# Kernel optimization log

Measured on AMD Instinct MI355X. Metric: run time of the kernel, lower is better.

## Reference

```python
import jax, jax.numpy as jnp
import numpy as np

_SAMPLING_EPS = 1e-05
_RMAX = 0.9999999403953552          # largest float32 uniform from tl.rand
_RMAX_LOG = -5.960464477539063e-08  # log(_RMAX)


def setup_inputs() -> dict:
    key = jax.random.key(0)
    k1, k2, k3, k4, k5 = jax.random.split(key, 5)
    B, V = 256, 128000
    logits = jax.random.normal(k1, (B, V), dtype=jnp.float32) * 4.0
    temperature = jax.random.uniform(k2, (B,), dtype=jnp.float32, minval=0.1, maxval=1.5)
    top_k = jax.random.randint(k3, (B,), 1, 1000).astype(jnp.int32)
    top_p = jax.random.uniform(k4, (B,), dtype=jnp.float32, minval=0.5, maxval=1.0)
    gumbel_u = jax.random.uniform(k5, (B, V), dtype=jnp.float32)
    return {
        "logits": logits,
        "temperature": temperature,
        "top_k": top_k,
        "top_p": top_p,
        "gumbel_u": gumbel_u,
        "num_logprobs": 20,
    }


def reference(logits, temperature, top_k, top_p, gumbel_u, num_logprobs):
    B, V = logits.shape
    # --- apply_temperature: divide by temp, temp<eps treated as 1.0 (greedy) ---
    temp = jnp.where(temperature < _SAMPLING_EPS, 1.0, temperature)
    logits = logits.astype(jnp.float32) / temp[:, None]

    # --- apply_top_k_top_p: sort ascending, mask, scatter back ---
    idx_sort = jnp.argsort(logits, axis=-1)                      # ascending
    logits_sort = jnp.take_along_axis(logits, idx_sort, axis=-1)
    # top-k: value of the k-th largest is at position V-k in ascending order
    k_pos = (V - top_k.astype(jnp.int32))[:, None]
    thresh = jnp.take_along_axis(logits_sort, k_pos, axis=-1)    # [B,1]
    logits_sort = jnp.where(logits_sort < thresh, -jnp.inf, logits_sort)
    # top-p: drop ascending prefix whose cumulative prob <= 1-p (keep last)
    probs_sort = jax.nn.softmax(logits_sort, axis=-1)
    cum = jnp.cumsum(probs_sort, axis=-1)
    mask_p = cum <= (1.0 - top_p)[:, None]
    mask_p = mask_p.at[:, -1].set(False)
    logits_sort = jnp.where(mask_p, -jnp.inf, logits_sort)
    # unsort back to vocab order
    inv = jnp.argsort(idx_sort, axis=-1)
    logits_f = jnp.take_along_axis(logits_sort, inv, axis=-1)

    # --- softmax + gumbel-trick sampling: argmax(p / -log(u)) ---
    probs = jax.nn.softmax(logits_f, axis=-1)
    q = -jnp.where(gumbel_u >= _RMAX, _RMAX_LOG, jnp.log(gumbel_u))
    greedy = (temperature < _SAMPLING_EPS)[:, None]  # kernel skips these rows
    ratio = jnp.where(greedy, probs, probs / q)
    sampled = jnp.argmax(ratio, axis=-1)             # [B]

    # --- gather_logprobs ---
    logprobs = jax.nn.log_softmax(logits_f, axis=-1)
    sampled_lp = jnp.take_along_axis(logprobs, sampled[:, None], axis=-1)  # [B,1]
    ranks = jnp.sum(logprobs > sampled_lp, axis=-1)                        # [B]
    topk_lp, topk_idx = jax.lax.top_k(logprobs, num_logprobs)
    indices = jnp.concatenate([sampled[:, None], topk_idx], axis=1)        # [B,1+K]
    lp_vals = jnp.concatenate([sampled_lp, topk_lp], axis=1)               # [B,1+K]

    return sampled[:, None], indices, lp_vals, ranks
```

## Files before the change

kernel.cpp:

```cpp
#include <hip/hip_runtime.h>
#include <math.h>

#define NTHR 1024
#define CAP 4096
#define BINS 4096

#define RMAX_F 0.9999999403953552f
#define RMAX_LOG_F -5.960464477539063e-08f
#define NEG_BIG -3.0e38f

__device__ __forceinline__ unsigned keyOf(float v) {
    unsigned b = __float_as_uint(v);
    return (b & 0x80000000u) ? ~b : (b | 0x80000000u);
}
__device__ __forceinline__ float valOfKey(unsigned k) {
    unsigned b = (k & 0x80000000u) ? (k ^ 0x80000000u) : ~k;
    return __uint_as_float(b);
}

__global__ __launch_bounds__(NTHR) void sampler_kernel(
    const float* __restrict__ logits,
    const float* __restrict__ temperature,
    const int* __restrict__ top_kv,
    const float* __restrict__ top_pv,
    const float* __restrict__ gumbel,
    float* __restrict__ out,
    int B, int V, int K)
{
    const int r = blockIdx.x;
    const int tid = threadIdx.x;
    const int lane = tid & 63;

    __shared__ unsigned long long cand[CAP];
    __shared__ int scanI[NTHR];
    __shared__ float varr[1024];
    __shared__ float Earr[1024];
    __shared__ float sfx[1024];
    __shared__ unsigned char flagArr[1024];
    __shared__ unsigned bitmap[64];
    __shared__ unsigned s_tlo;
    __shared__ int s_fallback;
    __shared__ unsigned s_prefix;
    __shared__ int s_cntgt, s_total, s_lvl;
    __shared__ int s_ncand, s_nkeep, s_rank, s_g0, s_g1;
    __shared__ unsigned long long s_amax;
    __shared__ float s_vs;

    unsigned* hist = (unsigned*)cand;

    const float* row = logits + (long long)r * V;
    const float* urow = gumbel + (long long)r * V;

    float traw = temperature[r];
    bool greedy = traw < 1e-5f;
    float t = greedy ? 1.0f : traw;
    int k = top_kv[r];
    if (k < 1) k = 1;
    if (k > V) k = V;
    float p = top_pv[r];

    const float4* row4 = (const float4*)row;
    const int V4 = V >> 2;
    const int Vt = V4 << 2;
    const unsigned cpy = tid & 1u;

    auto procF4 = [&](float4 l4, int i4) {
        float vv[4] = { l4.x, l4.y, l4.z, l4.w };
        #pragma unroll
        for (int j = 0; j < 4; ++j) {
            unsigned key = keyOf(vv[j]);
            bool pred = (key >= s_tlo);
            unsigned long long mask = __ballot(pred ? 1 : 0);
            if (mask) {
                int leader = __ffsll(mask) - 1;
                int cnt = __popcll(mask);
                int base = 0;
                if (lane == leader) base = atomicAdd(&s_ncand, cnt);
                base = __shfl(base, leader);
                if (pred) {
                    int pos = base + __popcll(mask & ((1ULL << lane) - 1ULL));
                    if (pos < CAP) {
                        unsigned gidx = (unsigned)(i4 * 4 + j);
                        cand[pos] = ((unsigned long long)key << 32) | (unsigned)(~gidx);
                    }
                }
            }
        }
    };
    auto compact = [&]() {
        int i = tid;
        for (; i + 3 * NTHR < V4; i += 4 * NTHR) {
            float4 a0 = row4[i];
            float4 a1 = row4[i + NTHR];
            float4 a2 = row4[i + 2 * NTHR];
            float4 a3 = row4[i + 3 * NTHR];
            procF4(a0, i); procF4(a1, i + NTHR);
            procF4(a2, i + 2 * NTHR); procF4(a3, i + 3 * NTHR);
        }
        for (; i < V4; i += NTHR) { float4 a = row4[i]; procF4(a, i); }
        for (int j = Vt + tid; j < V; j += NTHR) {
            unsigned key = keyOf(row[j]);
            bool pred = (key >= s_tlo);
            unsigned long long mask = __ballot(pred ? 1 : 0);
            if (mask) {
                int leader = __ffsll(mask) - 1;
                int cnt = __popcll(mask);
                int base = 0;
                if (lane == leader) base = atomicAdd(&s_ncand, cnt);
                base = __shfl(base, leader);
                if (pred) {
                    int pos = base + __popcll(mask & ((1ULL << lane) - 1ULL));
                    if (pos < CAP)
                        cand[pos] = ((unsigned long long)key << 32) | (unsigned)(~(unsigned)j);
                }
            }
        }
    };

    for (int i = tid; i < BINS * 2; i += NTHR) hist[i] = 0;
    __syncthreads();
    for (int i = tid; i < V4; i += NTHR * 8) {
        float4 l4 = row4[i];
        atomicAdd(&hist[((keyOf(l4.x) >> 20) << 1) | cpy], 1u);
        atomicAdd(&hist[((keyOf(l4.y) >> 20) << 1) | cpy], 1u);
        atomicAdd(&hist[((keyOf(l4.z) >> 20) << 1) | cpy], 1u);
        atomicAdd(&hist[((keyOf(l4.w) >> 20) << 1) | cpy], 1u);
    }
    __syncthreads();
    {
        int base = tid << 2;
        int cs = 0;
        #pragma unroll
        for (int j = 0; j < 4; ++j)
            cs += (int)(hist[(base + j) * 2] + hist[(base + j) * 2 + 1]);
        scanI[tid] = cs;
    }
    __syncthreads();
    for (int d = 1; d < NTHR; d <<= 1) {
        int v = (tid + d < NTHR) ? scanI[tid + d] : 0;
        __syncthreads();
        scanI[tid] += v;
        __syncthreads();
    }
    const int S = scanI[0];
    long long ks = ((long long)k * S) / V;
    const int starg = (int)ks + 40 + (int)(ks >> 2);
    if (tid == 0) s_fallback = (2 * starg > S) ? 1 : 0;
    __syncthreads();
    if (!s_fallback) {
        int mine = scanI[tid];
        int above = (tid + 1 < NTHR) ? scanI[tid + 1] : 0;
        if (mine >= starg && above < starg) {
            int base = tid << 2;
            int run = above;
            for (int b = base + 3; b >= base; --b) {
                int mb = (int)(hist[b * 2] + hist[b * 2 + 1]);
                if (run + mb >= starg) { s_tlo = (unsigned)b << 20; break; }
                run += mb;
            }
        }
        __syncthreads();
        if (tid == 0) s_ncand = 0;
        __syncthreads();
        compact();
        __syncthreads();
        if (tid == 0) s_fallback = (s_ncand < k || s_ncand > CAP) ? 1 : 0;
    }
    __syncthreads();

    if (s_fallback) {
        for (int i = tid; i < BINS * 2; i += NTHR) hist[i] = 0;
        __syncthreads();
        for (int i = tid; i < V4; i += NTHR) {
            float4 l4 = row4[i];
            atomicAdd(&hist[((keyOf(l4.x) >> 20) << 1) | cpy], 1u);
            atomicAdd(&hist[((keyOf(l4.y) >> 20) << 1) | cpy], 1u);
            atomicAdd(&hist[((keyOf(l4.z) >> 20) << 1) | cpy], 1u);
            atomicAdd(&hist[((keyOf(l4.w) >> 20) << 1) | cpy], 1u);
        }
        for (int i = Vt + tid; i < V; i += NTHR)
            atomicAdd(&hist[((keyOf(row[i]) >> 20) << 1) | cpy], 1u);
        __syncthreads();
        {
            int base = tid << 2;
            int cs = 0;
            #pragma unroll
            for (int j = 0; j < 4; ++j)
                cs += (int)(hist[(base + j) * 2] + hist[(base + j) * 2 + 1]);
            scanI[tid] = cs;
        }
        __syncthreads();
        for (int d = 1; d < NTHR; d <<= 1) {
            int v = (tid + d < NTHR) ? scanI[tid + d] : 0;
            __syncthreads();
            scanI[tid] += v;
            __syncthreads();
        }
        {
            int mine = scanI[tid];
            int above = (tid + 1 < NTHR) ? scanI[tid + 1] : 0;
            if (mine >= k && above < k) {
                int base = tid << 2;
                int run = above;
                for (int b = base + 3; b >= base; --b) {
                    int mb = (int)(hist[b * 2] + hist[b * 2 + 1]);
                    if (run + mb >= k) {
                        s_prefix = (unsigned)b; s_cntgt = run;
                        s_total = run + mb; s_lvl = 0;
                        break;
                    }
                    run += mb;
                }
            }
        }
        for (int level = 1; level <= 2; ++level) {
            __syncthreads();
            if (s_total <= CAP) break;
            for (int i = tid; i < 512; i += NTHR) hist[i] = 0;
            __syncthreads();
            unsigned pfx = s_prefix;
            const int msh = 32 - (12 + 8 * (level - 1));
            const int bsh = msh - 8;
            for (int i = tid; i < V4; i += NTHR) {
                float4 l4 = row4[i];
                float vv[4] = { l4.x, l4.y, l4.z, l4.w };
                #pragma unroll
                for (int j = 0; j < 4; ++j) {
                    unsigned key = keyOf(vv[j]);
                    if ((key >> msh) == pfx)
                        atomicAdd(&hist[(((key >> bsh) & 255u) << 1) | cpy], 1u);
                }
            }
            for (int i = Vt + tid; i < V; i += NTHR) {
                unsigned key = keyOf(row[i]);
                if ((key >> msh) == pfx)
                    atomicAdd(&hist[(((key >> bsh) & 255u) << 1) | cpy], 1u);
            }
            __syncthreads();
            if (tid == 0) {
                int run = s_cntgt;
                for (int b = 255; b >= 0; --b) {
                    int mb = (int)(hist[b * 2] + hist[b * 2 + 1]);
                    if (run + mb >= k) {
                        s_prefix = (pfx << 8) | (unsigned)b;
                        s_cntgt = run; s_total = run + mb;
                        break;
                    }
                    run += mb;
                }
                s_lvl = level;
            }
        }
        __syncthreads();
        if (tid == 0) { s_tlo = s_prefix << (20 - 8 * s_lvl); s_ncand = 0; }
        __syncthreads();
        compact();
        __syncthreads();
    }

    int ncand = s_ncand; if (ncand > CAP) ncand = CAP;
    if (k > ncand) k = ncand;

    int P = 2; while (P < ncand) P <<= 1;
    for (int i = ncand + tid; i < P; i += NTHR) cand[i] = 0ULL;
    __syncthreads();
    for (int size = 2; size <= P; size <<= 1) {
        for (int stride = size >> 1; stride > 0; stride >>= 1) {
            for (int i = tid; i < P; i += NTHR) {
                int j = i ^ stride;
                if (j > i) {
                    unsigned long long a = cand[i], b = cand[j];
                    bool up = ((i & size) == 0);
                    bool sw = up ? (a < b) : (a > b);
                    if (sw) { cand[i] = b; cand[j] = a; }
                }
            }
            __syncthreads();
        }
    }

    for (int i = tid; i < 1024; i += NTHR)
        varr[i] = (i < ncand) ? (valOfKey((unsigned)(cand[i] >> 32)) / t) : NEG_BIG;
    __syncthreads();

    const float m = varr[0];
    const float tkeyV = varr[k - 1];
    int ntop = k;
    while (ntop < ncand) {
        float vi = (ntop < 1024) ? varr[ntop]
                                 : (valOfKey((unsigned)(cand[ntop] >> 32)) / t);
        if (vi != tkeyV) break;
        ++ntop;
    }
    if (ntop > 1024) ntop = 1024;

    for (int i = tid; i < 1024; i += NTHR) {
        float e = (i < ntop) ? expf(varr[i] - m) : 0.0f;
        Earr[i] = e;
        sfx[i] = e;
    }
    __syncthreads();
    for (int d = 1; d < 1024; d <<= 1) {
        float t0 = (tid + d < 1024) ? sfx[tid + d] : 0.0f;
        __syncthreads();
        sfx[tid] += t0;
        __syncthreads();
    }
    const float Zp = sfx[0];
    const float cmp = 1.0f - p;
    if (tid == 0) { s_nkeep = 0; s_rank = 0; s_amax = 0ULL; }
    for (int i = tid; i < 64; i += NTHR) bitmap[i] = 0;
    __syncthreads();
    {
        int local = 0;
        for (int i = tid; i < ntop; i += NTHR)
            if (sfx[i] / Zp > cmp) local++;
        if (local) atomicAdd(&s_nkeep, local);
    }
    __syncthreads();
    const int nkeep = s_nkeep;
    if (tid == 0) {
        float vb = varr[nkeep - 1];
        int g0 = nkeep - 1;
        while (g0 > 0 && varr[g0 - 1] == vb) --g0;
        int g1 = nkeep;
        while (g1 < ntop && varr[g1] == vb) ++g1;
        s_g0 = g0; s_g1 = g1;
    }
    __syncthreads();
    const int g0 = s_g0, g1 = s_g1;
    const int mkeep = nkeep - g0;
    for (int i = g0 + tid; i < g1; i += NTHR) {
        unsigned gi = ~(unsigned)(cand[i] & 0xFFFFFFFFull);
        int rk = 0;
        for (int j = g0; j < g1; ++j) {
            unsigned gj = ~(unsigned)(cand[j] & 0xFFFFFFFFull);
            if (gj > gi) rk++;
        }
        flagArr[i] = (rk < mkeep) ? 1 : 0;
    }
    __syncthreads();

    const float Z2 = (nkeep < 1024) ? (Zp - sfx[nkeep]) : Zp;
    const float L = logf(Z2);

    for (int i = tid; i < g1; i += NTHR) {
        if (i < g0 || flagArr[i]) {
            unsigned lo = (unsigned)(cand[i] & 0xFFFFFFFFull);
            unsigned gidx = ~lo;
            float u = urow[gidx];
            float q = -((u >= RMAX_F) ? RMAX_LOG_F : logf(u));
            float prob = Earr[i] / Z2;
            float ratio = greedy ? prob : (prob / q);
            unsigned long long comp = ((unsigned long long)__float_as_uint(ratio) << 32) | lo;
            atomicMax(&s_amax, comp);
            if (gidx < 2048) atomicOr(&bitmap[gidx >> 5], 1u << (gidx & 31));
        }
    }
    __syncthreads();
    const unsigned samp_lo = (unsigned)(s_amax & 0xFFFFFFFFull);
    const unsigned samp = ~samp_lo;
    for (int i = tid; i < ntop; i += NTHR)
        if ((unsigned)(cand[i] & 0xFFFFFFFFull) == samp_lo) s_vs = varr[i];
    __syncthreads();
    const float lp_s = (s_vs - m) - L;
    {
        int local = 0;
        for (int i = tid; i < nkeep; i += NTHR)
            if ((varr[i] - m) - L > lp_s) local++;
        if (local) atomicAdd(&s_rank, local);
    }
    __syncthreads();

    if (tid == 0) {
        float* o_samp = out;
        float* o_idx  = out + B;
        float* o_lp   = out + B + (long long)B * (K + 1);
        float* o_rank = out + B + 2LL * B * (K + 1);
        long long rowo = (long long)r * (K + 1);

        o_samp[r] = (float)samp;
        o_idx[rowo] = (float)samp;
        o_lp[rowo] = lp_s;
        o_rank[r] = (float)s_rank;

        int ntk = (nkeep < K) ? nkeep : K;
        int slot = 0, i = 0;
        while (slot < ntk && i < g1) {
            float v = varr[i];
            int re = i + 1;
            while (re < g1 && varr[re] == v) ++re;
            long long last = -1;
            while (slot < ntk) {
                unsigned best = 0xFFFFFFFFu;
                for (int j = i; j < re; ++j) {
                    if (j >= g0 && !flagArr[j]) continue;
                    unsigned gj = ~(unsigned)(cand[j] & 0xFFFFFFFFull);
                    if ((long long)gj > last && gj < best) best = gj;
                }
                if (best == 0xFFFFFFFFu) break;
                o_idx[rowo + 1 + slot] = (float)best;
                o_lp[rowo + 1 + slot] = (v - m) - L;
                last = best; ++slot;
            }
            i = re;
        }
        if (nkeep < K) {
            int j = 0;
            for (int c = nkeep; c < K; ++c) {
                while (bitmap[j >> 5] & (1u << (j & 31))) ++j;
                o_idx[rowo + 1 + c] = (float)j;
                o_lp[rowo + 1 + c] = NEG_BIG;
                ++j;
            }
        }
    }
}

extern "C" void kernel_launch(void* const* d_in, const int* in_sizes, int n_in,
                              void* d_out, int out_size, void* d_ws, size_t ws_size,
                              hipStream_t stream) {
    const float* logits      = (const float*)d_in[0];
    const float* temperature = (const float*)d_in[1];
    const int*   top_k       = (const int*)d_in[2];
    const float* top_p       = (const float*)d_in[3];
    const float* gumbel      = (const float*)d_in[4];
    int B = in_sizes[1];
    int V = in_sizes[0] / B;
    int K = (out_size / B - 4) / 2;
    sampler_kernel<<<B, NTHR, 0, stream>>>(logits, temperature, top_k, top_p,
                                           gumbel, (float*)d_out, B, V, K);
}
```

Before: 323.2 us.

## Split sampler into threshold, multi-block compaction, and final kernels

Splits the single per-row kernel into three launches: a sampled histogram that estimates a per-row threshold, a candidate compaction spread over 8 blocks per row that writes to a global workspace through global atomics, and a final kernel that loads the candidates and does the sort, top-p, sampling and logprobs. The goal is to parallelise the full-row scan, which dominates the time, across more blocks than the 256 rows provide, so more CUs stream memory at once. It adds two extra launches, workspace traffic and global atomics, and falls back to the in-block path when the workspace is too small or the candidate count is off.

```diff
diff --git a/kernel.cpp b/kernel.cpp
--- a/kernel.cpp
+++ b/kernel.cpp
@@ -1,9 +1,12 @@
 #include <hip/hip_runtime.h>
 #include <math.h>
 
-#define NTHR 1024
+#define BINS 4096
 #define CAP 4096
-#define BINS 4096
+#define G 8
+#define NT1 1024
+#define NT2 256
+#define NT3 1024
 
 #define RMAX_F 0.9999999403953552f
 #define RMAX_LOG_F -5.960464477539063e-08f
@@ -18,28 +21,151 @@
     return __uint_as_float(b);
 }
 
-__global__ __launch_bounds__(NTHR) void sampler_kernel(
+__global__ __launch_bounds__(NT1) void k_thresh(
+    const float* __restrict__ logits, const int* __restrict__ top_kv,
+    unsigned* __restrict__ tloA, int* __restrict__ cntA, int V)
+{
+    const int r = blockIdx.x;
+    const int tid = threadIdx.x;
+    __shared__ unsigned hist[BINS * 2];
+    __shared__ int scanI[NT1];
+    __shared__ unsigned s_tlo;
+
+    const float* row = logits + (long long)r * V;
+    int k = top_kv[r];
+    if (k < 1) k = 1;
+    if (k > V) k = V;
+    const float4* row4 = (const float4*)row;
+    const int V4 = V >> 2;
+    const unsigned cpy = tid & 1u;
+
+    for (int i = tid; i < BINS * 2; i += NT1) hist[i] = 0;
+    if (tid == 0) s_tlo = 0u;
+    __syncthreads();
+    for (int i = tid; i < V4; i += NT1 * 8) {
+        float4 l4 = row4[i];
+        atomicAdd(&hist[((keyOf(l4.x) >> 20) << 1) | cpy], 1u);
+        atomicAdd(&hist[((keyOf(l4.y) >> 20) << 1) | cpy], 1u);
+        atomicAdd(&hist[((keyOf(l4.z) >> 20) << 1) | cpy], 1u);
+        atomicAdd(&hist[((keyOf(l4.w) >> 20) << 1) | cpy], 1u);
+    }
+    __syncthreads();
+    {
+        int base = tid << 2;
+        int cs = 0;
+        #pragma unroll
+        for (int j = 0; j < 4; ++j)
+            cs += (int)(hist[(base + j) * 2] + hist[(base + j) * 2 + 1]);
+        scanI[tid] = cs;
+    }
+    __syncthreads();
+    for (int d = 1; d < NT1; d <<= 1) {
+        int v = (tid + d < NT1) ? scanI[tid + d] : 0;
+        __syncthreads();
+        scanI[tid] += v;
+        __syncthreads();
+    }
+    const int S = scanI[0];
+    long long ks = ((long long)k * S) / V;
+    const int starg = (int)ks + 40 + (int)(ks >> 2);
+    const bool ok = (starg >= 1) && (2 * starg <= S);
+    if (ok) {
+        int mine = scanI[tid];
+        int above = (tid + 1 < NT1) ? scanI[tid + 1] : 0;
+        if (mine >= starg && above < starg) {
+            int base = tid << 2;
+            int run = above;
+            for (int b = base + 3; b >= base; --b) {
+                int mb = (int)(hist[b * 2] + hist[b * 2 + 1]);
+                if (run + mb >= starg) { s_tlo = (unsigned)b << 20; break; }
+                run += mb;
+            }
+        }
+    }
+    __syncthreads();
+    if (tid == 0) { tloA[r] = s_tlo; cntA[r] = 0; }
+}
+
+__global__ __launch_bounds__(NT2) void k_compact(
+    const float* __restrict__ logits, const unsigned* __restrict__ tloA,
+    int* __restrict__ cntA, unsigned long long* __restrict__ candg,
+    int V, int capws)
+{
+    const int gb = blockIdx.x;
+    const int r = gb >> 3;
+    const int s = gb & 7;
+    const int tid = threadIdx.x;
+    const int lane = tid & 63;
+
+    const float* row = logits + (long long)r * V;
+    const unsigned tlo = tloA[r];
+    int* cnt = &cntA[r];
+    unsigned long long* cbase = candg + (long long)r * capws;
+    const float4* row4 = (const float4*)row;
+    const int V4 = V >> 2;
+    const int Vt = V4 << 2;
+
+    auto emit = [&](unsigned key, unsigned gidx) {
+        bool pred = (key >= tlo);
+        unsigned long long mask = __ballot(pred ? 1 : 0);
+        if (mask) {
+            int leader = __ffsll(mask) - 1;
+            int c = __popcll(mask);
+            int base = 0;
+            if (lane == leader) base = atomicAdd(cnt, c);
+            base = __shfl(base, leader);
+            if (pred) {
+                int pos = base + __popcll(mask & ((1ULL << lane) - 1ULL));
+                if (pos < capws)
+                    cbase[pos] = ((unsigned long long)key << 32) | (unsigned)(~gidx);
+            }
+        }
+    };
+    auto procF4 = [&](float4 l4, int i4) {
+        emit(keyOf(l4.x), (unsigned)(i4 * 4 + 0));
+        emit(keyOf(l4.y), (unsigned)(i4 * 4 + 1));
+        emit(keyOf(l4.z), (unsigned)(i4 * 4 + 2));
+        emit(keyOf(l4.w), (unsigned)(i4 * 4 + 3));
+    };
+
+    const int stride = NT2 * G;
+    int i = s * NT2 + tid;
+    for (; i + 3 * stride < V4; i += 4 * stride) {
+        float4 a0 = row4[i];
+        float4 a1 = row4[i + stride];
+        float4 a2 = row4[i + 2 * stride];
+        float4 a3 = row4[i + 3 * stride];
+        procF4(a0, i); procF4(a1, i + stride);
+        procF4(a2, i + 2 * stride); procF4(a3, i + 3 * stride);
+    }
+    for (; i < V4; i += stride) { float4 a = row4[i]; procF4(a, i); }
+    if (s == 0)
+        for (int j = Vt + tid; j < V; j += NT2) emit(keyOf(row[j]), (unsigned)j);
+}
+
+__global__ __launch_bounds__(NT3) void k_final(
     const float* __restrict__ logits,
     const float* __restrict__ temperature,
     const int* __restrict__ top_kv,
     const float* __restrict__ top_pv,
     const float* __restrict__ gumbel,
+    const unsigned long long* __restrict__ candg,
+    const int* __restrict__ cntA,
     float* __restrict__ out,
-    int B, int V, int K)
+    int B, int V, int K, int capws)
 {
     const int r = blockIdx.x;
     const int tid = threadIdx.x;
     const int lane = tid & 63;
 
     __shared__ unsigned long long cand[CAP];
-    __shared__ int scanI[NTHR];
+    __shared__ int scanI[NT3];
     __shared__ float varr[1024];
     __shared__ float Earr[1024];
     __shared__ float sfx[1024];
     __shared__ unsigned char flagArr[1024];
     __shared__ unsigned bitmap[64];
     __shared__ unsigned s_tlo;
-    __shared__ int s_fallback;
     __shared__ unsigned s_prefix;
     __shared__ int s_cntgt, s_total, s_lvl;
     __shared__ int s_ncand, s_nkeep, s_rank, s_g0, s_g1;
@@ -64,41 +190,125 @@
     const int Vt = V4 << 2;
     const unsigned cpy = tid & 1u;
 
-    auto procF4 = [&](float4 l4, int i4) {
-        float vv[4] = { l4.x, l4.y, l4.z, l4.w };
-        #pragma unroll
-        for (int j = 0; j < 4; ++j) {
-            unsigned key = keyOf(vv[j]);
-            bool pred = (key >= s_tlo);
-            unsigned long long mask = __ballot(pred ? 1 : 0);
-            if (mask) {
-                int leader = __ffsll(mask) - 1;
-                int cnt = __popcll(mask);
-                int base = 0;
-                if (lane == leader) base = atomicAdd(&s_ncand, cnt);
-                base = __shfl(base, leader);
-                if (pred) {
-                    int pos = base + __popcll(mask & ((1ULL << lane) - 1ULL));
-                    if (pos < CAP) {
-                        unsigned gidx = (unsigned)(i4 * 4 + j);
-                        cand[pos] = ((unsigned long long)key << 32) | (unsigned)(~gidx);
+    const int ncand0 = cntA[r];
+    const bool fb = (ncand0 < k) || (ncand0 > capws);
+    int ncand;
+
+    if (!fb) {
+        const unsigned long long* cbase = candg + (long long)r * capws;
+        for (int i = tid; i < ncand0; i += NT3) cand[i] = cbase[i];
+        ncand = ncand0;
+    } else {
+        for (int i = tid; i < BINS * 2; i += NT3) hist[i] = 0;
+        __syncthreads();
+        for (int i = tid; i < V4; i += NT3) {
+            float4 l4 = row4[i];
+            atomicAdd(&hist[((keyOf(l4.x) >> 20) << 1) | cpy], 1u);
+            atomicAdd(&hist[((keyOf(l4.y) >> 20) << 1) | cpy], 1u);
+            atomicAdd(&hist[((keyOf(l4.z) >> 20) << 1) | cpy], 1u);
+            atomicAdd(&hist[((keyOf(l4.w) >> 20) << 1) | cpy], 1u);
+        }
+        for (int i = Vt + tid; i < V; i += NT3)
+            atomicAdd(&hist[((keyOf(row[i]) >> 20) << 1) | cpy], 1u);
+        __syncthreads();
+        {
+            int base = tid << 2;
+            int cs = 0;
+            #pragma unroll
+            for (int j = 0; j < 4; ++j)
+                cs += (int)(hist[(base + j) * 2] + hist[(base + j) * 2 + 1]);
+            scanI[tid] = cs;
+        }
+        __syncthreads();
+        for (int d = 1; d < NT3; d <<= 1) {
+            int v = (tid + d < NT3) ? scanI[tid + d] : 0;
+            __syncthreads();
+            scanI[tid] += v;
+            __syncthreads();
+        }
+        {
+            int mine = scanI[tid];
+            int above = (tid + 1 < NT3) ? scanI[tid + 1] : 0;
+            if (mine >= k && above < k) {
+                int base = tid << 2;
+                int run = above;
+                for (int b = base + 3; b >= base; --b) {
+                    int mb = (int)(hist[b * 2] + hist[b * 2 + 1]);
+                    if (run + mb >= k) {
+                        s_prefix = (unsigned)b; s_cntgt = run;
+                        s_total = run + mb; s_lvl = 0;
+                        break;
                     }
-                }
-            }
-        }
-    };
-    auto compact = [&]() {
-        int i = tid;
-        for (; i + 3 * NTHR < V4; i += 4 * NTHR) {
-            float4 a0 = row4[i];
-            float4 a1 = row4[i + NTHR];
-            float4 a2 = row4[i + 2 * NTHR];
-            float4 a3 = row4[i + 3 * NTHR];
-            procF4(a0, i); procF4(a1, i + NTHR);
-            procF4(a2, i + 2 * NTHR); procF4(a3, i + 3 * NTHR);
-        }
-        for (; i < V4; i += NTHR) { float4 a = row4[i]; procF4(a, i); }
-        for (int j = Vt + tid; j < V; j += NTHR) {
+                    run += mb;
+                }
+            }
+        }
+        for (int level = 1; level <= 2; ++level) {
+            __syncthreads();
+            if (s_total <= CAP) break;
+            for (int i = tid; i < 512; i += NT3) hist[i] = 0;
+            __syncthreads();
+            unsigned pfx = s_prefix;
+            const int msh = 32 - (12 + 8 * (level - 1));
+            const int bsh = msh - 8;
+            for (int i = tid; i < V4; i += NT3) {
+                float4 l4 = row4[i];
+                float vv[4] = { l4.x, l4.y, l4.z, l4.w };
+                #pragma unroll
+                for (int j = 0; j < 4; ++j) {
+                    unsigned key = keyOf(vv[j]);
+                    if ((key >> msh) == pfx)
+                        atomicAdd(&hist[(((key >> bsh) & 255u) << 1) | cpy], 1u);
+                }
+            }
+            for (int i = Vt + tid; i < V; i += NT3) {
+                unsigned key = keyOf(row[i]);
+                if ((key >> msh) == pfx)
+                    atomicAdd(&hist[(((key >> bsh) & 255u) << 1) | cpy], 1u);
+            }
+            __syncthreads();
+            if (tid == 0) {
+                int run = s_cntgt;
+                for (int b = 255; b >= 0; --b) {
+                    int mb = (int)(hist[b * 2] + hist[b * 2 + 1]);
+                    if (run + mb >= k) {
+                        s_prefix = (pfx << 8) | (unsigned)b;
+                        s_cntgt = run; s_total = run + mb;
+                        break;
+                    }
+                    run += mb;
+                }
+                s_lvl = level;
+            }
+        }
+        __syncthreads();
+        if (tid == 0) { s_tlo = s_prefix << (20 - 8 * s_lvl); s_ncand = 0; }
+        __syncthreads();
+        for (int i = tid; i < V4; i += NT3) {
+            float4 l4 = row4[i];
+            float vv[4] = { l4.x, l4.y, l4.z, l4.w };
+            #pragma unroll
+            for (int j = 0; j < 4; ++j) {
+                unsigned key = keyOf(vv[j]);
+                bool pred = (key >= s_tlo);
+                unsigned long long mask = __ballot(pred ? 1 : 0);
+                if (mask) {
+                    int leader = __ffsll(mask) - 1;
+                    int cnt = __popcll(mask);
+                    int base = 0;
+                    if (lane == leader) base = atomicAdd(&s_ncand, cnt);
+                    base = __shfl(base, leader);
+                    if (pred) {
+                        int pos = base + __popcll(mask & ((1ULL << lane) - 1ULL));
+                        if (pos < CAP) {
+                            unsigned gidx = (unsigned)(i * 4 + j);
+                            cand[pos] = ((unsigned long long)key << 32) | (unsigned)(~gidx);
+                        }
+                    }
+                }
+            }
+        }
+        for (int j = Vt + tid; j < V; j += NT3) {
             unsigned key = keyOf(row[j]);
             bool pred = (key >= s_tlo);
             unsigned long long mask = __ballot(pred ? 1 : 0);
@@ -115,158 +325,18 @@
                 }
             }
         }
-    };
-
-    for (int i = tid; i < BINS * 2; i += NTHR) hist[i] = 0;
-    __syncthreads();
-    for (int i = tid; i < V4; i += NTHR * 8) {
-        float4 l4 = row4[i];
-        atomicAdd(&hist[((keyOf(l4.x) >> 20) << 1) | cpy], 1u);
-        atomicAdd(&hist[((keyOf(l4.y) >> 20) << 1) | cpy], 1u);
-        atomicAdd(&hist[((keyOf(l4.z) >> 20) << 1) | cpy], 1u);
-        atomicAdd(&hist[((keyOf(l4.w) >> 20) << 1) | cpy], 1u);
-    }
-    __syncthreads();
-    {
-        int base = tid << 2;
-        int cs = 0;
-        #pragma unroll
-        for (int j = 0; j < 4; ++j)
-            cs += (int)(hist[(base + j) * 2] + hist[(base + j) * 2 + 1]);
-        scanI[tid] = cs;
-    }
-    __syncthreads();
-    for (int d = 1; d < NTHR; d <<= 1) {
-        int v = (tid + d < NTHR) ? scanI[tid + d] : 0;
-        __syncthreads();
-        scanI[tid] += v;
-        __syncthreads();
-    }
-    const int S = scanI[0];
-    long long ks = ((long long)k * S) / V;
-    const int starg = (int)ks + 40 + (int)(ks >> 2);
-    if (tid == 0) s_fallback = (2 * starg > S) ? 1 : 0;
-    __syncthreads();
-    if (!s_fallback) {
-        int mine = scanI[tid];
-        int above = (tid + 1 < NTHR) ? scanI[tid + 1] : 0;
-        if (mine >= starg && above < starg) {
-            int base = tid << 2;
-            int run = above;
-            for (int b = base + 3; b >= base; --b) {
-                int mb = (int)(hist[b * 2] + hist[b * 2 + 1]);
-                if (run + mb >= starg) { s_tlo = (unsigned)b << 20; break; }
-                run += mb;
-            }
-        }
-        __syncthreads();
-        if (tid == 0) s_ncand = 0;
-        __syncthreads();
-        compact();
-        __syncthreads();
-        if (tid == 0) s_fallback = (s_ncand < k || s_ncand > CAP) ? 1 : 0;
-    }
-    __syncthreads();
-
-    if (s_fallback) {
-        for (int i = tid; i < BINS * 2; i += NTHR) hist[i] = 0;
-        __syncthreads();
-        for (int i = tid; i < V4; i += NTHR) {
-            float4 l4 = row4[i];
-            atomicAdd(&hist[((keyOf(l4.x) >> 20) << 1) | cpy], 1u);
-            atomicAdd(&hist[((keyOf(l4.y) >> 20) << 1) | cpy], 1u);
-            atomicAdd(&hist[((keyOf(l4.z) >> 20) << 1) | cpy], 1u);
-            atomicAdd(&hist[((keyOf(l4.w) >> 20) << 1) | cpy], 1u);
-        }
-        for (int i = Vt + tid; i < V; i += NTHR)
-            atomicAdd(&hist[((keyOf(row[i]) >> 20) << 1) | cpy], 1u);
-        __syncthreads();
-        {
-            int base = tid << 2;
-            int cs = 0;
-            #pragma unroll
-            for (int j = 0; j < 4; ++j)
-                cs += (int)(hist[(base + j) * 2] + hist[(base + j) * 2 + 1]);
-            scanI[tid] = cs;
-        }
-        __syncthreads();
-        for (int d = 1; d < NTHR; d <<= 1) {
-            int v = (tid + d < NTHR) ? scanI[tid + d] : 0;
-            __syncthreads();
-            scanI[tid] += v;
-            __syncthreads();
-        }
-        {
-            int mine = scanI[tid];
-            int above = (tid + 1 < NTHR) ? scanI[tid + 1] : 0;
-            if (mine >= k && above < k) {
-                int base = tid << 2;
-                int run = above;
-                for (int b = base + 3; b >= base; --b) {
-                    int mb = (int)(hist[b * 2] + hist[b * 2 + 1]);
-                    if (run + mb >= k) {
-                        s_prefix = (unsigned)b; s_cntgt = run;
-                        s_total = run + mb; s_lvl = 0;
-                        break;
-                    }
-                    run += mb;
-                }
-            }
-        }
-        for (int level = 1; level <= 2; ++level) {
-            __syncthreads();
-            if (s_total <= CAP) break;
-            for (int i = tid; i < 512; i += NTHR) hist[i] = 0;
-            __syncthreads();
-            unsigned pfx = s_prefix;
-            const int msh = 32 - (12 + 8 * (level - 1));
-            const int bsh = msh - 8;
-            for (int i = tid; i < V4; i += NTHR) {
-                float4 l4 = row4[i];
-                float vv[4] = { l4.x, l4.y, l4.z, l4.w };
-                #pragma unroll
-                for (int j = 0; j < 4; ++j) {
-                    unsigned key = keyOf(vv[j]);
-                    if ((key >> msh) == pfx)
-                        atomicAdd(&hist[(((key >> bsh) & 255u) << 1) | cpy], 1u);
-                }
-            }
-            for (int i = Vt + tid; i < V; i += NTHR) {
-                unsigned key = keyOf(row[i]);
-                if ((key >> msh) == pfx)
-                    atomicAdd(&hist[(((key >> bsh) & 255u) << 1) | cpy], 1u);
-            }
-            __syncthreads();
-            if (tid == 0) {
-                int run = s_cntgt;
-                for (int b = 255; b >= 0; --b) {
-                    int mb = (int)(hist[b * 2] + hist[b * 2 + 1]);
-                    if (run + mb >= k) {
-                        s_prefix = (pfx << 8) | (unsigned)b;
-                        s_cntgt = run; s_total = run + mb;
-                        break;
-                    }
-                    run += mb;
-                }
-                s_lvl = level;
-            }
-        }
-        __syncthreads();
-        if (tid == 0) { s_tlo = s_prefix << (20 - 8 * s_lvl); s_ncand = 0; }
-        __syncthreads();
-        compact();
-        __syncthreads();
-    }
-
-    int ncand = s_ncand; if (ncand > CAP) ncand = CAP;
-    if (k > ncand) k = ncand;
+        __syncthreads();
+        ncand = s_ncand; if (ncand > CAP) ncand = CAP;
+        if (k > ncand) k = ncand;
+    }
+    __syncthreads();
 
     int P = 2; while (P < ncand) P <<= 1;
-    for (int i = ncand + tid; i < P; i += NTHR) cand[i] = 0ULL;
+    for (int i = ncand + tid; i < P; i += NT3) cand[i] = 0ULL;
     __syncthreads();
     for (int size = 2; size <= P; size <<= 1) {
         for (int stride = size >> 1; stride > 0; stride >>= 1) {
-            for (int i = tid; i < P; i += NTHR) {
+            for (int i = tid; i < P; i += NT3) {
                 int j = i ^ stride;
                 if (j > i) {
                     unsigned long long a = cand[i], b = cand[j];
@@ -279,7 +349,7 @@
         }
     }
 
-    for (int i = tid; i < 1024; i += NTHR)
+    for (int i = tid; i < 1024; i += NT3)
         varr[i] = (i < ncand) ? (valOfKey((unsigned)(cand[i] >> 32)) / t) : NEG_BIG;
     __syncthreads();
 
@@ -294,7 +364,7 @@
     }
     if (ntop > 1024) ntop = 1024;
 
-    for (int i = tid; i < 1024; i += NTHR) {
+    for (int i = tid; i < 1024; i += NT3) {
         float e = (i < ntop) ? expf(varr[i] - m) : 0.0f;
         Earr[i] = e;
         sfx[i] = e;
@@ -309,11 +379,11 @@
     const float Zp = sfx[0];
     const float cmp = 1.0f - p;
     if (tid == 0) { s_nkeep = 0; s_rank = 0; s_amax = 0ULL; }
-    for (int i = tid; i < 64; i += NTHR) bitmap[i] = 0;
+    for (int i = tid; i < 64; i += NT3) bitmap[i] = 0;
     __syncthreads();
     {
         int local = 0;
-        for (int i = tid; i < ntop; i += NTHR)
+        for (int i = tid; i < ntop; i += NT3)
             if (sfx[i] / Zp > cmp) local++;
         if (local) atomicAdd(&s_nkeep, local);
     }
@@ -330,7 +400,7 @@
     __syncthreads();
     const int g0 = s_g0, g1 = s_g1;
     const int mkeep = nkeep - g0;
-    for (int i = g0 + tid; i < g1; i += NTHR) {
+    for (int i = g0 + tid; i < g1; i += NT3) {
         unsigned gi = ~(unsigned)(cand[i] & 0xFFFFFFFFull);
         int rk = 0;
         for (int j = g0; j < g1; ++j) {
@@ -344,7 +414,7 @@
     const float Z2 = (nkeep < 1024) ? (Zp - sfx[nkeep]) : Zp;
     const float L = logf(Z2);
 
-    for (int i = tid; i < g1; i += NTHR) {
+    for (int i = tid; i < g1; i += NT3) {
         if (i < g0 || flagArr[i]) {
             unsigned lo = (unsigned)(cand[i] & 0xFFFFFFFFull);
             unsigned gidx = ~lo;
@@ -360,13 +430,13 @@
     __syncthreads();
     const unsigned samp_lo = (unsigned)(s_amax & 0xFFFFFFFFull);
     const unsigned samp = ~samp_lo;
-    for (int i = tid; i < ntop; i += NTHR)
+    for (int i = tid; i < ntop; i += NT3)
         if ((unsigned)(cand[i] & 0xFFFFFFFFull) == samp_lo) s_vs = varr[i];
     __syncthreads();
     const float lp_s = (s_vs - m) - L;
     {
         int local = 0;
-        for (int i = tid; i < nkeep; i += NTHR)
+        for (int i = tid; i < nkeep; i += NT3)
             if ((varr[i] - m) - L > lp_s) local++;
         if (local) atomicAdd(&s_rank, local);
     }
@@ -428,6 +498,18 @@
     int B = in_sizes[1];
     int V = in_sizes[0] / B;
     int K = (out_size / B - 4) / 2;
-    sampler_kernel<<<B, NTHR, 0, stream>>>(logits, temperature, top_k, top_p,
-                                           gumbel, (float*)d_out, B, V, K);
+
+    int* cntA = (int*)d_ws;
+    unsigned* tloA = (unsigned*)((char*)d_ws + (size_t)B * 4);
+    size_t candOff = ((size_t)B * 8 + 7) & ~(size_t)7;
+    size_t candBytes = (ws_size > candOff) ? (ws_size - candOff) : 0;
+    int capws = (int)(candBytes / (8ull * (size_t)B));
+    if (capws > CAP) capws = CAP;
+    if (capws < 0) capws = 0;
+    unsigned long long* candg = (unsigned long long*)((char*)d_ws + candOff);
+
+    k_thresh<<<B, NT1, 0, stream>>>(logits, top_k, tloA, cntA, V);
+    k_compact<<<B * G, NT2, 0, stream>>>(logits, tloA, cntA, candg, V, capws);
+    k_final<<<B, NT3, 0, stream>>>(logits, temperature, top_k, top_p, gumbel,
+                                   candg, cntA, (float*)d_out, B, V, K, capws);
 }
```

Measured after the change: 585.0 us. 81.0% more time.
